# Optimization experiments

Hardware: AMD Instinct MI355X
Metric: run time of the kernel (lower is better)

Reference implementation:

```python
import jax, jax.numpy as jnp
import numpy as np

N_NODES = 100000
N_EDGES = 1250000
IN_DIM = 128
HID = 64


def gcn_conv(x, W, b, src, dst, n_nodes):
    # PyG GCNConv: h = D^{-1/2} (A + I) D^{-1/2} (X W) + b
    h = x @ W  # [N, out]
    loop = jnp.arange(n_nodes)
    s = jnp.concatenate([src, loop])
    d = jnp.concatenate([dst, loop])
    deg = jnp.zeros((n_nodes,), h.dtype).at[d].add(1.0)
    dinv = jnp.where(deg > 0, deg ** -0.5, 0.0)
    norm = dinv[s] * dinv[d]  # [E+N]
    msgs = h[s] * norm[:, None]  # irregular gather, memory-bound
    out = jax.ops.segment_sum(msgs, d, num_segments=n_nodes)
    return out + b


def setup_inputs() -> dict:
    key = jax.random.key(0)
    ks = jax.random.split(key, 4)
    x = jax.random.normal(ks[0], (N_NODES, IN_DIM), jnp.float32)
    edge_index = jax.random.randint(ks[1], (2, N_EDGES), 0, N_NODES, jnp.int64)
    # Glorot-ish init for linear weights
    W1 = jax.random.normal(ks[2], (IN_DIM, HID), jnp.float32) * (1.0 / np.sqrt(IN_DIM))
    b1 = jnp.zeros((HID,), jnp.float32)
    W2 = jax.random.normal(ks[3], (HID, HID), jnp.float32) * (1.0 / np.sqrt(HID))
    b2 = jnp.zeros((HID,), jnp.float32)
    return {"x": x, "edge_index": edge_index, "W1": W1, "b1": b1, "W2": W2, "b2": b2}


def reference(x, edge_index, W1, b1, W2, b2):
    n_nodes = x.shape[0]
    src, dst = edge_index[0], edge_index[1]
    h = gcn_conv(x, W1, b1, src, dst, n_nodes)
    h = jax.nn.relu(h)  # dropout is identity in eval mode
    h = gcn_conv(h, W2, b2, src, dst, n_nodes)
    return h
```

## Files before the change

### kernel.cpp

```cpp
#include <hip/hip_runtime.h>
#include <hip/hip_fp16.h>

constexpr int NN = 100000;
constexpr int NE = 1250000;
constexpr int KDIM = 128;
constexpr int HID = 64;

constexpr int NPB = 128;
constexpr int NB  = (NN + NPB - 1) / NPB;
constexpr int NBP = 1024;
constexpr int CAP = 2048;
constexpr int BIN_BLOCKS = 256;
constexpr int BIN_CHUNK  = (NE + BIN_BLOCKS - 1) / BIN_BLOCKS;
constexpr int EPT = (BIN_CHUNK + 1023) / 1024;

using half8   = __attribute__((ext_vector_type(8))) _Float16;
using floatx4 = __attribute__((ext_vector_type(4))) float;

__global__ __launch_bounds__(256) void k_prep(const float* __restrict__ W1,
                                              const float* __restrict__ W2,
                                              __half* __restrict__ Whp1,
                                              __half* __restrict__ Whp2,
                                              int* __restrict__ gcur) {
    const int blk = blockIdx.x;
    if (blk < 4) {
        int t = blk * 256 + threadIdx.x;
        int lane = t & 63, frag = t >> 6;
        int ks = frag >> 2, ct = frag & 3;
        int quad = lane >> 4, n = lane & 15;
        __half tmp[8];
#pragma unroll
        for (int j = 0; j < 8; ++j)
            tmp[j] = __float2half(W1[(ks * 32 + quad * 8 + j) * HID + ct * 16 + n]);
        *(uint4*)(Whp1 + t * 8) = *(uint4*)tmp;
    } else if (blk < 6) {
        int t = (blk - 4) * 256 + threadIdx.x;
        int lane = t & 63, frag = t >> 6;
        int ks = frag >> 2, ct = frag & 3;
        int quad = lane >> 4, n = lane & 15;
        __half tmp[8];
#pragma unroll
        for (int j = 0; j < 8; ++j)
            tmp[j] = __float2half(W2[(ks * 32 + quad * 8 + j) * HID + ct * 16 + n]);
        *(uint4*)(Whp2 + t * 8) = *(uint4*)tmp;
    } else {
        for (int i = threadIdx.x; i < NBP; i += 256) gcur[i] = 0;
    }
}

__global__ __launch_bounds__(1024) void k_bin(const int* __restrict__ src,
                                              const int* __restrict__ dst,
                                              int* __restrict__ gcur,
                                              unsigned* __restrict__ pack1) {
    __shared__ int cnt[NBP], rnk[NBP], gbase[NBP];
    const int t = threadIdx.x;
    for (int i = t; i < NBP; i += 1024) { cnt[i] = 0; rnk[i] = 0; }
    __syncthreads();
    const int c0 = blockIdx.x * BIN_CHUNK;
    int b[EPT];
    unsigned val[EPT];
#pragma unroll
    for (int i = 0; i < EPT; ++i) {
        int idx = i * 1024 + t;
        int e = c0 + idx;
        b[i] = -1;
        if (idx < BIN_CHUNK && e < NE) {
            int d = dst[e], s = src[e];
            int bb = d >> 7;
            b[i] = bb;
            val[i] = (unsigned)s | ((unsigned)(d & 127) << 17);
            atomicAdd(&cnt[bb], 1);
        }
    }
    __syncthreads();
    for (int i = t; i < NBP; i += 1024) {
        int c = cnt[i];
        if (c) gbase[i] = i * CAP + atomicAdd(&gcur[i], c);
    }
    __syncthreads();
#pragma unroll
    for (int i = 0; i < EPT; ++i) {
        if (b[i] >= 0) {
            int r = atomicAdd(&rnk[b[i]], 1);
            pack1[gbase[b[i]] + r] = val[i];
        }
    }
}

__global__ __launch_bounds__(256) void k_sort(const unsigned* __restrict__ pack1,
                                              const int* __restrict__ gcur,
                                              unsigned* __restrict__ pack2,
                                              int* __restrict__ row_start,
                                              int* __restrict__ deg,
                                              float* __restrict__ dinv) {
    __shared__ int h[NPB];
    __shared__ int sh[NPB];
    const int t = threadIdx.x;
    const int bkt = blockIdx.x;
    if (t < NPB) h[t] = 0;
    __syncthreads();
    const int beg = bkt * CAP, end = beg + gcur[bkt];
    for (int i = beg + t; i < end; i += 256)
        atomicAdd(&h[(pack1[i] >> 17) & 127], 1);
    __syncthreads();
    int v0 = 0;
    if (t < NPB) { v0 = h[t]; sh[t] = v0; }
    __syncthreads();
    int val = v0;
    for (int off = 1; off < NPB; off <<= 1) {
        int add = (t < NPB && t >= off) ? sh[t - off] : 0;
        __syncthreads();
        if (t < NPB) { val += add; sh[t] = val; }
        __syncthreads();
    }
    if (t < NPB) {
        int start = beg + (val - v0);
        int node = bkt * NPB + t;
        if (node < NN) {
            row_start[node] = start;
            deg[node] = v0;
            dinv[node] = rsqrtf((float)(v0 + 1));
        }
        h[t] = start;
    }
    __syncthreads();
    for (int i = beg + t; i < end; i += 256) {
        unsigned p = pack1[i];
        int pos = atomicAdd(&h[(p >> 17) & 127], 1);
        pack2[pos] = p & 0x1FFFF;
    }
}

template <int K>
__global__ __launch_bounds__(256) void k_mm(const float* __restrict__ x,
                                            const __half* __restrict__ Whp,
                                            const float* __restrict__ dinv,
                                            __half* __restrict__ gout) {
    const int t = threadIdx.x;
    const int w = t >> 6, lane = t & 63;
    const int quad = lane >> 4, m = lane & 15;
    const int rowA = blockIdx.x * 64 + w * 16 + m;
    const bool rok = rowA < NN;
    const float* xr = x + (long)rowA * K + quad * 8;

    floatx4 acc[4] = {};
#pragma unroll
    for (int ks = 0; ks < K / 32; ++ks) {
        float xv[8];
        if (rok) {
            float4 p0 = *(const float4*)(xr + ks * 32);
            float4 p1 = *(const float4*)(xr + ks * 32 + 4);
            xv[0] = p0.x; xv[1] = p0.y; xv[2] = p0.z; xv[3] = p0.w;
            xv[4] = p1.x; xv[5] = p1.y; xv[6] = p1.z; xv[7] = p1.w;
        } else {
#pragma unroll
            for (int j = 0; j < 8; ++j) xv[j] = 0.f;
        }
        half8 a;
#pragma unroll
        for (int j = 0; j < 8; ++j) a[j] = (_Float16)xv[j];
#pragma unroll
        for (int ct = 0; ct < 4; ++ct) {
            half8 b = *(const half8*)(Whp + ((ks * 4 + ct) * 64 + lane) * 8);
            acc[ct] = __builtin_amdgcn_mfma_f32_16x16x32_f16(a, b, acc[ct], 0, 0, 0);
        }
    }

#pragma unroll
    for (int r = 0; r < 4; ++r) {
        int rowD = blockIdx.x * 64 + w * 16 + quad * 4 + r;
        if (rowD < NN) {
            float dv = dinv[rowD];
#pragma unroll
            for (int ct = 0; ct < 4; ++ct)
                gout[rowD * HID + ct * 16 + m] = __float2half(dv * acc[ct][r]);
        }
    }
}

__global__ __launch_bounds__(256) void k_aggmm(const unsigned* __restrict__ pack2,
                                               const int* __restrict__ row_start,
                                               const int* __restrict__ deg,
                                               const float* __restrict__ dinv,
                                               const __half* __restrict__ g1,
                                               const float* __restrict__ b1,
                                               const __half* __restrict__ Whp2,
                                               __half* __restrict__ g2) {
    __shared__ __half tile[16][72];
    const int w = threadIdx.x >> 6, lane = threadIdx.x & 63;
    const int sub = lane & 15, slot = lane >> 4;
    const int vbase = blockIdx.x * 16 + w * 4;
    const float4 bv = *(const float4*)(b1 + sub * 4);

#pragma unroll
    for (int i = 0; i < 4; ++i) {
        const int v = vbase + i;
        const int beg = row_start[v];
        const int cnt = deg[v];
        int pre = 0;
        if (lane < cnt) pre = (int)pack2[beg + lane];
        const int n0 = cnt < 64 ? cnt : 64;
        float4 acc = make_float4(0.f, 0.f, 0.f, 0.f);

        int k = 0;
        for (; k + 8 <= n0; k += 8) {
            int sA = __shfl(pre, k + slot);
            int sB = __shfl(pre, k + 4 + slot);
            uint2 rA = *(const uint2*)(g1 + sA * HID + sub * 4);
            uint2 rB = *(const uint2*)(g1 + sB * HID + sub * 4);
            float2 a0 = __half22float2(*(const __half2*)&rA.x);
            float2 a1 = __half22float2(*(const __half2*)&rA.y);
            float2 b0 = __half22float2(*(const __half2*)&rB.x);
            float2 b1f = __half22float2(*(const __half2*)&rB.y);
            acc.x += a0.x + b0.x; acc.y += a0.y + b0.y;
            acc.z += a1.x + b1f.x; acc.w += a1.y + b1f.y;
        }
        for (; k < n0; k += 4) {
            int idx  = k + slot;
            int idxc = idx < n0 ? idx : 0;
            int s = __shfl(pre, idxc);
            if (idx < n0) {
                uint2 r = *(const uint2*)(g1 + s * HID + sub * 4);
                float2 a0 = __half22float2(*(const __half2*)&r.x);
                float2 a1 = __half22float2(*(const __half2*)&r.y);
                acc.x += a0.x; acc.y += a0.y; acc.z += a1.x; acc.w += a1.y;
            }
        }
        for (int kk = 64 + slot; kk < cnt; kk += 4) {
            int s = (int)pack2[beg + kk];
            uint2 r = *(const uint2*)(g1 + s * HID + sub * 4);
            float2 a0 = __half22float2(*(const __half2*)&r.x);
            float2 a1 = __half22float2(*(const __half2*)&r.y);
            acc.x += a0.x; acc.y += a0.y; acc.z += a1.x; acc.w += a1.y;
        }
#pragma unroll
        for (int mm = 16; mm <= 32; mm <<= 1) {
            acc.x += __shfl_xor(acc.x, mm);
            acc.y += __shfl_xor(acc.y, mm);
            acc.z += __shfl_xor(acc.z, mm);
            acc.w += __shfl_xor(acc.w, mm);
        }
        if (slot == 0) {
            const float dv = dinv[v];
            uint2 sr = *(const uint2*)(g1 + v * HID + sub * 4);
            float2 s0 = __half22float2(*(const __half2*)&sr.x);
            float2 s1 = __half22float2(*(const __half2*)&sr.y);
            __half tmp[4];
            tmp[0] = __float2half(fmaxf(dv * (acc.x + s0.x) + bv.x, 0.f));
            tmp[1] = __float2half(fmaxf(dv * (acc.y + s0.y) + bv.y, 0.f));
            tmp[2] = __float2half(fmaxf(dv * (acc.z + s1.x) + bv.z, 0.f));
            tmp[3] = __float2half(fmaxf(dv * (acc.w + s1.y) + bv.w, 0.f));
            *(uint2*)&tile[w * 4 + i][sub * 4] = *(uint2*)tmp;
        }
    }
    __syncthreads();

    const int quad = slot, m = sub;
    floatx4 acc2 = {};
#pragma unroll
    for (int ks = 0; ks < 2; ++ks) {
        half8 a = *(const half8*)&tile[m][ks * 32 + quad * 8];
        half8 b = *(const half8*)(Whp2 + ((ks * 4 + w) * 64 + lane) * 8);
        acc2 = __builtin_amdgcn_mfma_f32_16x16x32_f16(a, b, acc2, 0, 0, 0);
    }
#pragma unroll
    for (int r = 0; r < 4; ++r) {
        int rowD = blockIdx.x * 16 + quad * 4 + r;
        g2[rowD * HID + w * 16 + m] = __float2half(dinv[rowD] * acc2[r]);
    }
}

__global__ __launch_bounds__(256) void k_agg(const unsigned* __restrict__ pack2,
                                             const int* __restrict__ row_start,
                                             const int* __restrict__ deg,
                                             const float* __restrict__ dinv,
                                             const __half* __restrict__ g,
                                             const float* __restrict__ bias,
                                             float* __restrict__ out) {
    const int v = blockIdx.x * 4 + (threadIdx.x >> 6);
    if (v >= NN) return;
    const int lane = threadIdx.x & 63;
    const int sub  = lane & 15;
    const int slot = lane >> 4;
    const int beg = row_start[v];
    const int cnt = deg[v];
    int pre = 0;
    if (lane < cnt) pre = (int)pack2[beg + lane];
    const int n0 = cnt < 64 ? cnt : 64;
    float4 acc = make_float4(0.f, 0.f, 0.f, 0.f);

    int k = 0;
    for (; k + 8 <= n0; k += 8) {
        int sA = __shfl(pre, k + slot);
        int sB = __shfl(pre, k + 4 + slot);
        uint2 rA = *(const uint2*)(g + sA * HID + sub * 4);
        uint2 rB = *(const uint2*)(g + sB * HID + sub * 4);
        float2 a0 = __half22float2(*(const __half2*)&rA.x);
        float2 a1 = __half22float2(*(const __half2*)&rA.y);
        float2 b0 = __half22float2(*(const __half2*)&rB.x);
        float2 b1 = __half22float2(*(const __half2*)&rB.y);
        acc.x += a0.x + b0.x; acc.y += a0.y + b0.y;
        acc.z += a1.x + b1.x; acc.w += a1.y + b1.y;
    }
    for (; k < n0; k += 4) {
        int idx  = k + slot;
        int idxc = idx < n0 ? idx : 0;
        int s = __shfl(pre, idxc);
        if (idx < n0) {
            uint2 r = *(const uint2*)(g + s * HID + sub * 4);
            float2 a0 = __half22float2(*(const __half2*)&r.x);
            float2 a1 = __half22float2(*(const __half2*)&r.y);
            acc.x += a0.x; acc.y += a0.y; acc.z += a1.x; acc.w += a1.y;
        }
    }
    for (int kk = 64 + slot; kk < cnt; kk += 4) {
        int s = (int)pack2[beg + kk];
        uint2 r = *(const uint2*)(g + s * HID + sub * 4);
        float2 a0 = __half22float2(*(const __half2*)&r.x);
        float2 a1 = __half22float2(*(const __half2*)&r.y);
        acc.x += a0.x; acc.y += a0.y; acc.z += a1.x; acc.w += a1.y;
    }
#pragma unroll
    for (int mm = 16; mm <= 32; mm <<= 1) {
        acc.x += __shfl_xor(acc.x, mm);
        acc.y += __shfl_xor(acc.y, mm);
        acc.z += __shfl_xor(acc.z, mm);
        acc.w += __shfl_xor(acc.w, mm);
    }
    if (slot == 0) {
        const float dv = dinv[v];
        uint2 sr = *(const uint2*)(g + v * HID + sub * 4);
        float2 s0 = __half22float2(*(const __half2*)&sr.x);
        float2 s1 = __half22float2(*(const __half2*)&sr.y);
        float4 bv = *(const float4*)(bias + sub * 4);
        float4 o;
        o.x = dv * (acc.x + s0.x) + bv.x;
        o.y = dv * (acc.y + s0.y) + bv.y;
        o.z = dv * (acc.z + s1.x) + bv.z;
        o.w = dv * (acc.w + s1.y) + bv.w;
        *(float4*)(out + v * HID + sub * 4) = o;
    }
}

extern "C" void kernel_launch(void* const* d_in, const int* in_sizes, int n_in,
                              void* d_out, int out_size, void* d_ws, size_t ws_size,
                              hipStream_t stream) {
    const float* x  = (const float*)d_in[0];
    const int*   ei = (const int*)d_in[1];
    const float* W1 = (const float*)d_in[2];
    const float* b1 = (const float*)d_in[3];
    const float* W2 = (const float*)d_in[4];
    const float* b2 = (const float*)d_in[5];
    float* out = (float*)d_out;
    (void)in_sizes; (void)n_in; (void)out_size; (void)ws_size;

    const int* src = ei;
    const int* dst = ei + NE;

    char* ws = (char*)d_ws;
    int*      gcur      = (int*)(ws + 0x000000);
    __half*   Whp1      = (__half*)(ws + 0x004000);
    __half*   Whp2      = (__half*)(ws + 0x008000);
    float*    dinv      = (float*)(ws + 0x010000);
    int*      row_start = (int*)(ws + 0x080000);
    int*      deg       = (int*)(ws + 0x100000);
    unsigned* pack1     = (unsigned*)(ws + 0x200000);
    unsigned* pack2     = (unsigned*)(ws + 0xA00000);
    __half*   g1        = (__half*)(ws + 0x1200000);
    __half*   g2        = (__half*)(ws + 0x2000000);

    k_prep<<<7, 256, 0, stream>>>(W1, W2, Whp1, Whp2, gcur);
    k_bin<<<BIN_BLOCKS, 1024, 0, stream>>>(src, dst, gcur, pack1);
    k_sort<<<NB, 256, 0, stream>>>(pack1, gcur, pack2, row_start, deg, dinv);

    k_mm<KDIM><<<(NN + 63) / 64, 256, 0, stream>>>(x, Whp1, dinv, g1);
    k_aggmm<<<NN / 16, 256, 0, stream>>>(pack2, row_start, deg, dinv, g1, b1, Whp2, g2);
    k_agg<<<(NN + 3) / 4, 256, 0, stream>>>(pack2, row_start, deg, dinv, g2, b2, out);
}
```

Baseline: 211.6 us.

## Split layer-2 features into two column halves and aggregate each separately

The second-layer transformed features are now written as two 32-column half arrays, and the final aggregation runs twice, once per half, with 8 lanes per row and 8 edges per pass. Each half table is 6.4 MB instead of 12.8 MB, so the random gathers are meant to hit cache more often. The cost is reading the CSR indices twice and an extra kernel launch. k_aggmm also preloads row_start, deg, dinv and the neighbor indices for all four of its nodes before starting the gathers.

Measured after the change: 237.1 us. 1.12x slower.

```diff
diff --git a/kernel.cpp b/kernel.cpp
--- a/kernel.cpp
+++ b/kernel.cpp
@@ -185,27 +185,39 @@
                                                const __half* __restrict__ g1,
                                                const float* __restrict__ b1,
                                                const __half* __restrict__ Whp2,
-                                               __half* __restrict__ g2) {
+                                               __half* __restrict__ g2a,
+                                               __half* __restrict__ g2b) {
     __shared__ __half tile[16][72];
     const int w = threadIdx.x >> 6, lane = threadIdx.x & 63;
     const int sub = lane & 15, slot = lane >> 4;
     const int vbase = blockIdx.x * 16 + w * 4;
     const float4 bv = *(const float4*)(b1 + sub * 4);
 
+    int4   rs4 = *(const int4*)(row_start + vbase);
+    int4   dg4 = *(const int4*)(deg + vbase);
+    float4 dv4 = *(const float4*)(dinv + vbase);
+    const int   beg_i[4] = {rs4.x, rs4.y, rs4.z, rs4.w};
+    const int   cnt_i[4] = {dg4.x, dg4.y, dg4.z, dg4.w};
+    const float dv_i[4]  = {dv4.x, dv4.y, dv4.z, dv4.w};
+    int pre[4];
+#pragma unroll
+    for (int i = 0; i < 4; ++i) {
+        pre[i] = 0;
+        if (lane < cnt_i[i]) pre[i] = (int)pack2[beg_i[i] + lane];
+    }
+
 #pragma unroll
     for (int i = 0; i < 4; ++i) {
         const int v = vbase + i;
-        const int beg = row_start[v];
-        const int cnt = deg[v];
-        int pre = 0;
-        if (lane < cnt) pre = (int)pack2[beg + lane];
+        const int beg = beg_i[i];
+        const int cnt = cnt_i[i];
         const int n0 = cnt < 64 ? cnt : 64;
         float4 acc = make_float4(0.f, 0.f, 0.f, 0.f);
 
         int k = 0;
         for (; k + 8 <= n0; k += 8) {
-            int sA = __shfl(pre, k + slot);
-            int sB = __shfl(pre, k + 4 + slot);
+            int sA = __shfl(pre[i], k + slot);
+            int sB = __shfl(pre[i], k + 4 + slot);
             uint2 rA = *(const uint2*)(g1 + sA * HID + sub * 4);
             uint2 rB = *(const uint2*)(g1 + sB * HID + sub * 4);
             float2 a0 = __half22float2(*(const __half2*)&rA.x);
@@ -218,7 +230,7 @@
         for (; k < n0; k += 4) {
             int idx  = k + slot;
             int idxc = idx < n0 ? idx : 0;
-            int s = __shfl(pre, idxc);
+            int s = __shfl(pre[i], idxc);
             if (idx < n0) {
                 uint2 r = *(const uint2*)(g1 + s * HID + sub * 4);
                 float2 a0 = __half22float2(*(const __half2*)&r.x);
@@ -241,7 +253,7 @@
             acc.w += __shfl_xor(acc.w, mm);
         }
         if (slot == 0) {
-            const float dv = dinv[v];
+            const float dv = dv_i[i];
             uint2 sr = *(const uint2*)(g1 + v * HID + sub * 4);
             float2 s0 = __half22float2(*(const __half2*)&sr.x);
             float2 s1 = __half22float2(*(const __half2*)&sr.y);
@@ -255,7 +267,7 @@
     }
     __syncthreads();
 
-    const int quad = slot, m = sub;
+    const int quad = lane >> 4, m = lane & 15;
     floatx4 acc2 = {};
 #pragma unroll
     for (int ks = 0; ks < 2; ++ks) {
@@ -263,25 +275,28 @@
         half8 b = *(const half8*)(Whp2 + ((ks * 4 + w) * 64 + lane) * 8);
         acc2 = __builtin_amdgcn_mfma_f32_16x16x32_f16(a, b, acc2, 0, 0, 0);
     }
+    __half* gd = (w < 2) ? g2a : g2b;
+    const int c = (w & 1) * 16 + m;
 #pragma unroll
     for (int r = 0; r < 4; ++r) {
         int rowD = blockIdx.x * 16 + quad * 4 + r;
-        g2[rowD * HID + w * 16 + m] = __float2half(dinv[rowD] * acc2[r]);
-    }
-}
-
-__global__ __launch_bounds__(256) void k_agg(const unsigned* __restrict__ pack2,
-                                             const int* __restrict__ row_start,
-                                             const int* __restrict__ deg,
-                                             const float* __restrict__ dinv,
-                                             const __half* __restrict__ g,
-                                             const float* __restrict__ bias,
-                                             float* __restrict__ out) {
+        gd[rowD * 32 + c] = __float2half(dinv[rowD] * acc2[r]);
+    }
+}
+
+template <int H>
+__global__ __launch_bounds__(256) void k_aggH(const unsigned* __restrict__ pack2,
+                                              const int* __restrict__ row_start,
+                                              const int* __restrict__ deg,
+                                              const float* __restrict__ dinv,
+                                              const __half* __restrict__ gh,
+                                              const float* __restrict__ bias,
+                                              float* __restrict__ out) {
     const int v = blockIdx.x * 4 + (threadIdx.x >> 6);
     if (v >= NN) return;
     const int lane = threadIdx.x & 63;
-    const int sub  = lane & 15;
-    const int slot = lane >> 4;
+    const int sub  = lane & 7;
+    const int slot = lane >> 3;
     const int beg = row_start[v];
     const int cnt = deg[v];
     int pre = 0;
@@ -290,11 +305,11 @@
     float4 acc = make_float4(0.f, 0.f, 0.f, 0.f);
 
     int k = 0;
-    for (; k + 8 <= n0; k += 8) {
+    for (; k + 16 <= n0; k += 16) {
         int sA = __shfl(pre, k + slot);
-        int sB = __shfl(pre, k + 4 + slot);
-        uint2 rA = *(const uint2*)(g + sA * HID + sub * 4);
-        uint2 rB = *(const uint2*)(g + sB * HID + sub * 4);
+        int sB = __shfl(pre, k + 8 + slot);
+        uint2 rA = *(const uint2*)(gh + sA * 32 + sub * 4);
+        uint2 rB = *(const uint2*)(gh + sB * 32 + sub * 4);
         float2 a0 = __half22float2(*(const __half2*)&rA.x);
         float2 a1 = __half22float2(*(const __half2*)&rA.y);
         float2 b0 = __half22float2(*(const __half2*)&rB.x);
@@ -302,26 +317,26 @@
         acc.x += a0.x + b0.x; acc.y += a0.y + b0.y;
         acc.z += a1.x + b1.x; acc.w += a1.y + b1.y;
     }
-    for (; k < n0; k += 4) {
+    for (; k < n0; k += 8) {
         int idx  = k + slot;
         int idxc = idx < n0 ? idx : 0;
         int s = __shfl(pre, idxc);
         if (idx < n0) {
-            uint2 r = *(const uint2*)(g + s * HID + sub * 4);
+            uint2 r = *(const uint2*)(gh + s * 32 + sub * 4);
             float2 a0 = __half22float2(*(const __half2*)&r.x);
             float2 a1 = __half22float2(*(const __half2*)&r.y);
             acc.x += a0.x; acc.y += a0.y; acc.z += a1.x; acc.w += a1.y;
         }
     }
-    for (int kk = 64 + slot; kk < cnt; kk += 4) {
+    for (int kk = 64 + slot; kk < cnt; kk += 8) {
         int s = (int)pack2[beg + kk];
-        uint2 r = *(const uint2*)(g + s * HID + sub * 4);
+        uint2 r = *(const uint2*)(gh + s * 32 + sub * 4);
         float2 a0 = __half22float2(*(const __half2*)&r.x);
         float2 a1 = __half22float2(*(const __half2*)&r.y);
         acc.x += a0.x; acc.y += a0.y; acc.z += a1.x; acc.w += a1.y;
     }
 #pragma unroll
-    for (int mm = 16; mm <= 32; mm <<= 1) {
+    for (int mm = 8; mm <= 32; mm <<= 1) {
         acc.x += __shfl_xor(acc.x, mm);
         acc.y += __shfl_xor(acc.y, mm);
         acc.z += __shfl_xor(acc.z, mm);
@@ -329,16 +344,16 @@
     }
     if (slot == 0) {
         const float dv = dinv[v];
-        uint2 sr = *(const uint2*)(g + v * HID + sub * 4);
+        uint2 sr = *(const uint2*)(gh + v * 32 + sub * 4);
         float2 s0 = __half22float2(*(const __half2*)&sr.x);
         float2 s1 = __half22float2(*(const __half2*)&sr.y);
-        float4 bv = *(const float4*)(bias + sub * 4);
+        float4 bv = *(const float4*)(bias + H * 32 + sub * 4);
         float4 o;
         o.x = dv * (acc.x + s0.x) + bv.x;
         o.y = dv * (acc.y + s0.y) + bv.y;
         o.z = dv * (acc.z + s1.x) + bv.z;
         o.w = dv * (acc.w + s1.y) + bv.w;
-        *(float4*)(out + v * HID + sub * 4) = o;
+        *(float4*)(out + v * HID + H * 32 + sub * 4) = o;
     }
 }
 
@@ -367,13 +382,16 @@
     unsigned* pack1     = (unsigned*)(ws + 0x200000);
     unsigned* pack2     = (unsigned*)(ws + 0xA00000);
     __half*   g1        = (__half*)(ws + 0x1200000);
-    __half*   g2        = (__half*)(ws + 0x2000000);
+    __half*   g2a       = (__half*)(ws + 0x2000000);
+    __half*   g2b       = (__half*)(ws + 0x2800000);
 
     k_prep<<<7, 256, 0, stream>>>(W1, W2, Whp1, Whp2, gcur);
     k_bin<<<BIN_BLOCKS, 1024, 0, stream>>>(src, dst, gcur, pack1);
     k_sort<<<NB, 256, 0, stream>>>(pack1, gcur, pack2, row_start, deg, dinv);
 
     k_mm<KDIM><<<(NN + 63) / 64, 256, 0, stream>>>(x, Whp1, dinv, g1);
-    k_aggmm<<<NN / 16, 256, 0, stream>>>(pack2, row_start, deg, dinv, g1, b1, Whp2, g2);
-    k_agg<<<(NN + 3) / 4, 256, 0, stream>>>(pack2, row_start, deg, dinv, g2, b2, out);
-}
+    k_aggmm<<<NN / 16, 256, 0, stream>>>(pack2, row_start, deg, dinv, g1, b1, Whp2,
+                                         g2a, g2b);
+    k_aggH<0><<<(NN + 3) / 4, 256, 0, stream>>>(pack2, row_start, deg, dinv, g2a, b2, out);
+    k_aggH<1><<<(NN + 3) / 4, 256, 0, stream>>>(pack2, row_start, deg, dinv, g2b, b2, out);
+}
```
